# Performance work log

Hardware: AMD Instinct MI355X
Metric: run time of the kernel (lower is better)

Reference implementation:

```python
import jax, jax.numpy as jnp
import numpy as np
import math

# ---- config (YOLOv3 / 416, COCO) ----
ANCS_SCALE = np.array([[0.024,0.031],[0.038,0.072],[0.079,0.055],
                       [0.072,0.147],[0.149,0.108],[0.142,0.286],
                       [0.279,0.216],[0.375,0.476],[0.897,0.784]], dtype=np.float32)
NUMS_CENG = [2704, 676, 169]          # 52^2, 26^2, 13^2
NUMS_ANC = [3, 3, 3]
NUM_CLASSES = 80
LOSS_WEIGHT = [1.0, 1.0, 1.0]
B, NGT = 32, 20
HWA = sum(NUMS_CENG) * 3              # 10647
GDIM = 1 + NUM_CLASSES + 4 + 1 + 4    # conf + cls + txywh + weight + ltrb
FP16_EPS = 0.0009765625               # torch.finfo(float16).eps
BCE_EPS = 1e-6
GRIDS = [int(math.sqrt(n)) for n in NUMS_CENG]          # [52, 26, 13]
OFFS = [int(x) for x in np.cumsum([0] + NUMS_CENG)[:3]]  # layer offsets in cells


def ltrb2xywh(b):
    return jnp.concatenate([(b[..., :2] + b[..., 2:]) * 0.5, b[..., 2:] - b[..., :2]], axis=-1)


def x_bce(p, g):
    p = jnp.clip(p, BCE_EPS, 1.0 - BCE_EPS)
    return -(g * jnp.log(p) + (1.0 - g) * jnp.log(1.0 - p))


def fmatch4yolov3(gb_ltrb, glabels):
    """gb_ltrb [NGT,4] float, glabels [NGT] int -> g_yolo_one [HWA,GDIM].
    Faithful to the torch code, including the (buggy) inner loop over ALL
    GTs' best-anchor ids for each GT i, and the write order (-1 ignore first,
    positive row overwrite after), replicated via a sequential lax.scan."""
    ancs = jnp.asarray(ANCS_SCALE)
    gxywh = ltrb2xywh(gb_ltrb)
    wh = gxywh[:, 2:]                                     # [NGT,2]
    # wh-only IoU (boxes concentric at origin)
    inter = jnp.minimum(wh[:, None, 0], ancs[None, :, 0]) * jnp.minimum(wh[:, None, 1], ancs[None, :, 1])
    union = wh.prod(-1)[:, None] + ancs.prod(-1)[None, :] - inter
    ids_p_anc = jnp.argmax(inter / union, axis=-1).astype(jnp.int32)  # [NGT]
    weights = 2.0 - wh.prod(-1)
    onehot = jax.nn.one_hot(glabels - 1, NUM_CLASSES, dtype=gb_ltrb.dtype)
    g0 = jnp.zeros((HWA, GDIM), dtype=gb_ltrb.dtype)
    neg = jnp.full((3, 1), -1.0, dtype=gb_ltrb.dtype)

    def step(g, p):
        i = p // NGT            # GT whose cxy / wh / label are used
        k = p % NGT             # GT whose best anchor id is used
        cxy = gxywh[i, :2]
        a = ids_p_anc[k]
        ceng = a // NUMS_ANC[0]
        for j in range(3):      # static loop over the 3 layers
            grid, off = GRIDS[j], OFFS[j]
            colrow = (cxy * grid).astype(jnp.int32)       # [col,row]
            idx = (off + colrow[1] * grid + colrow[0]) * 3
            # ignore: conf=-1 for all 3 anchors of this cell
            g = jax.lax.dynamic_update_slice(g, neg, (idx, 0))
            # candidate positive row for this layer
            txy = (cxy - colrow.astype(cxy.dtype) / grid) * grid
            twh = jnp.log(wh[i] / ancs[a])
            t = jnp.concatenate([jnp.ones((1,), cxy.dtype), onehot[i], txy, twh,
                                 weights[i][None], gb_ltrb[i]])     # [GDIM]
            pidx = idx + (a % NUMS_ANC[j])
            cur = jax.lax.dynamic_slice(g, (pidx, 0), (1, GDIM))
            g = jax.lax.dynamic_update_slice(g, jnp.where(ceng == j, t[None, :], cur), (pidx, 0))
        return g, None

    g, _ = jax.lax.scan(step, g0, jnp.arange(NGT * NGT, dtype=jnp.int32))
    return g


def _forward(pconf, pcls, ptxywh, gboxes_ltrb, glabels):
    gyolos = jax.lax.stop_gradient(jax.vmap(fmatch4yolov3)(gboxes_ltrb, glabels))  # [B,HWA,GDIM]
    s_ = 1 + NUM_CLASSES
    gconf = gyolos[:, :, 0]
    mask_pos = (gconf > 0).astype(pconf.dtype)
    mask_neg = (gconf == 0).astype(pconf.dtype)
    nums_pos = jnp.clip(mask_pos.sum(-1), FP16_EPS, None)
    # cls loss (BCE on sigmoid, pos cells only)
    lv = x_bce(jax.nn.sigmoid(pcls), gyolos[:, :, 1:s_])
    l_cls = ((lv.sum(-1) * mask_pos).sum(-1) / nums_pos).mean() * LOSS_WEIGHT[2]
    # conf loss (MSE on sigmoid, masked means)
    pconf_sig = jax.nn.sigmoid(pconf).reshape(pconf.shape[0], -1)
    lv = (pconf_sig - gconf) ** 2
    l_conf_pos = (lv * mask_pos).sum() / mask_pos.sum() * LOSS_WEIGHT[0] * 30
    l_conf_neg = (lv * mask_neg).sum() / mask_neg.sum() * LOSS_WEIGHT[1] * 30
    # box loss: xy BCE, wh MSE, weighted by (2 - w*h)
    weight = gyolos[:, :, s_ + 4]
    lv = x_bce(jax.nn.sigmoid(ptxywh[:, :, :2]), gyolos[:, :, s_:s_ + 2])
    l_txty = ((lv.sum(-1) * mask_pos * weight).sum(-1) / nums_pos).mean()
    lv = (ptxywh[:, :, 2:4] - gyolos[:, :, s_ + 2:s_ + 4]) ** 2
    l_twth = ((lv.sum(-1) * mask_pos * weight).sum(-1) / nums_pos).mean()
    return l_conf_pos + l_conf_neg + l_cls + l_txty + l_twth


def setup_inputs() -> dict:
    key = jax.random.key(0)
    k1, k2, k3, k4, k5, k6 = jax.random.split(key, 6)
    pconf = jax.random.normal(k1, (B, HWA, 1), dtype=jnp.float32)
    pcls = jax.random.normal(k2, (B, HWA, NUM_CLASSES), dtype=jnp.float32)
    ptxywh = jax.random.normal(k3, (B, HWA, 4), dtype=jnp.float32)
    cxy = jax.random.uniform(k4, (B, NGT, 2), minval=0.2, maxval=0.8)
    wh = jax.random.uniform(k5, (B, NGT, 2), minval=0.05, maxval=0.3)
    gboxes_ltrb = jnp.concatenate([cxy - wh * 0.5, cxy + wh * 0.5], axis=-1)
    glabels = jax.random.randint(k6, (B, NGT), 1, NUM_CLASSES + 1, dtype=jnp.int32)
    return {"pconf": pconf, "pcls": pcls, "ptxywh": ptxywh,
            "gboxes_ltrb": gboxes_ltrb, "glabels": glabels}


def reference(pconf, pcls, ptxywh, gboxes_ltrb, glabels):
    return _forward(pconf, pcls, ptxywh, gboxes_ltrb, glabels)
```

## Files before the change

### kernel.cpp

```cpp
#include <hip/hip_runtime.h>
#include <math.h>

#define BATCH 32
#define NSLICE 16
#define SLICE_LEN 666
#define NGT 20
#define HWA 10647
#define NCLS 80
#define FP16_EPS 0.0009765625f
#define BCE_EPS 1e-6f

__device__ __constant__ float ANCS[9][2] = {
    {0.024f, 0.031f}, {0.038f, 0.072f}, {0.079f, 0.055f},
    {0.072f, 0.147f}, {0.149f, 0.108f}, {0.142f, 0.286f},
    {0.279f, 0.216f}, {0.375f, 0.476f}, {0.897f, 0.784f}};

__device__ __forceinline__ float flog(float x) { return __logf(x); }
__device__ __forceinline__ float fsig(float x) {
  return __builtin_amdgcn_rcpf(1.0f + __expf(-x));
}


__global__ __launch_bounds__(256) void yolo_main(
    const float* __restrict__ pconf,
    const float* __restrict__ pcls,
    const float* __restrict__ ptxywh,
    const float* __restrict__ gbox,
    const int* __restrict__ glab,
    float* __restrict__ part)
{
  const int b = blockIdx.x;
  const int sl = blockIdx.y;
  const int tid = threadIdx.x;
  const int r0 = sl * SLICE_LEN;
  const int r1 = min(r0 + SLICE_LEN, HWA);

  __shared__ int cell[SLICE_LEN];
  __shared__ int pos_list[256];
  __shared__ float s_cx[NGT], s_cy[NGT], s_w[NGT], s_h[NGT], s_wt[NGT];
  __shared__ int s_a[NGT], s_lab[NGT], s_idx[NGT][3];
  __shared__ int s_np;
  __shared__ float red[4][8];

  for (int r = tid; r < SLICE_LEN; r += 256) cell[r] = 0;
  if (tid == 0) s_np = 0;
  if (tid < NGT) {
    const float* gb = gbox + (b * NGT + tid) * 4;
    float l = gb[0], t = gb[1], r = gb[2], bo = gb[3];
    float cx = (l + r) * 0.5f, cy = (t + bo) * 0.5f;
    float w = r - l, h = bo - t;
    s_cx[tid] = cx; s_cy[tid] = cy; s_w[tid] = w; s_h[tid] = h;
    s_wt[tid] = 2.0f - w * h;
    s_lab[tid] = glab[b * NGT + tid];
    float best = -1e30f; int bi = 0;
    for (int a = 0; a < 9; ++a) {
      float inter = fminf(w, ANCS[a][0]) * fminf(h, ANCS[a][1]);
      float uni = w * h + ANCS[a][0] * ANCS[a][1] - inter;
      float ratio = inter / uni;
      if (ratio > best) { best = ratio; bi = a; }
    }
    s_a[tid] = bi;
    const int GR[3] = {52, 26, 13};
    const int OF[3] = {0, 2704, 3380};
    for (int j = 0; j < 3; ++j) {
      int col = (int)(cx * (float)GR[j]);
      int row = (int)(cy * (float)GR[j]);
      s_idx[tid][j] = (OF[j] + row * GR[j] + col) * 3;
    }
  }
  __syncthreads();

  for (int p = tid; p < NGT * NGT; p += 256) {
    int i = p / NGT, k = p - i * NGT;
    int a = s_a[k];
    int ceng = a / 3;
    int pn = (2 * p + 1) << 16;
    int pp = ((2 * p + 2) << 16) | (1 << 15) | (i * 9 + a);
    for (int j = 0; j < 3; ++j) {
      int idx = s_idx[i][j];
      if (idx + 2 >= r0 && idx < r1) {
#pragma unroll
        for (int d = 0; d < 3; ++d) {
          int t = idx + d;
          if (t >= r0 && t < r1) atomicMax(&cell[t - r0], pn);
        }
      }
      if (ceng == j) {
        int t = idx + (a - ceng * 3);
        if (t >= r0 && t < r1) atomicMax(&cell[t - r0], pp);
      }
    }
  }
  __syncthreads();

  float sum_pos = 0.f, sum_neg = 0.f;
  int cnt_pos = 0, cnt_neg = 0;
  for (int r = r0 + tid; r < r1; r += 256) {
    int c = cell[r - r0];
    float x = pconf[(size_t)b * HWA + r];
    float s = fsig(x);
    if (c == 0) {
      sum_neg += s * s; cnt_neg++;
    } else if (c & (1 << 15)) {
      float d = s - 1.0f; sum_pos += d * d; cnt_pos++;
      int slot = atomicAdd(&s_np, 1);
      if (slot < 256) pos_list[slot] = ((c & 0xFF) << 16) | r;
    }
  }
  __syncthreads();
  int P = s_np;

  float cls_sum = 0.f;
  for (int idx = tid; idx < P * NCLS; idx += 256) {
    int pr = idx / NCLS, c = idx - pr * NCLS;
    int pk = pos_list[pr];
    int r = pk & 0xFFFF, rec = pk >> 16;
    int i = rec / 9;
    int lab = s_lab[i] - 1;
    float x = pcls[((size_t)b * HWA + r) * NCLS + c];
    float s = fsig(x);
    s = fminf(fmaxf(s, BCE_EPS), 1.0f - BCE_EPS);
    float g = (c == lab) ? 1.0f : 0.0f;
    cls_sum += -(g * flog(s) + (1.0f - g) * flog(1.0f - s));
  }

  float txty_sum = 0.f, twth_sum = 0.f;
  for (int q = tid; q < P; q += 256) {
    int pk = pos_list[q];
    int r = pk & 0xFFFF, rec = pk >> 16;
    int i = rec / 9, a = rec - i * 9;
    int ceng = a / 3;
    const int GR[3] = {52, 26, 13};
    float grid = (float)GR[ceng];
    float cx = s_cx[i], cy = s_cy[i];
    int col = (int)(cx * grid), row = (int)(cy * grid);
    float tx = (cx - (float)col / grid) * grid;
    float ty = (cy - (float)row / grid) * grid;
    float twx = flog(s_w[i] / ANCS[a][0]);
    float twy = flog(s_h[i] / ANCS[a][1]);
    float wgt = s_wt[i];
    const float* pt = ptxywh + ((size_t)b * HWA + r) * 4;
    float s0 = fsig(pt[0]);
    float s1 = fsig(pt[1]);
    s0 = fminf(fmaxf(s0, BCE_EPS), 1.0f - BCE_EPS);
    s1 = fminf(fmaxf(s1, BCE_EPS), 1.0f - BCE_EPS);
    float b0 = -(tx * flog(s0) + (1.0f - tx) * flog(1.0f - s0));
    float b1 = -(ty * flog(s1) + (1.0f - ty) * flog(1.0f - s1));
    txty_sum += (b0 + b1) * wgt;
    float d2 = pt[2] - twx, d3 = pt[3] - twy;
    twth_sum += (d2 * d2 + d3 * d3) * wgt;
  }

  float v[7] = {sum_pos, sum_neg, cls_sum, txty_sum, twth_sum,
                (float)cnt_pos, (float)cnt_neg};
  int lane = tid & 63, wv = tid >> 6;
  for (int m = 0; m < 7; ++m) {
    float x = v[m];
    for (int o = 32; o > 0; o >>= 1) x += __shfl_down(x, o, 64);
    if (lane == 0) red[wv][m] = x;
  }
  __syncthreads();
  if (tid == 0) {
    float* w = part + (b * NSLICE + sl) * 8;
    for (int m = 0; m < 7; ++m)
      w[m] = red[0][m] + red[1][m] + red[2][m] + red[3][m];
  }
}

__global__ __launch_bounds__(512) void yolo_final(
    const float* __restrict__ part, float* __restrict__ out) {
  const int t = threadIdx.x;
  __shared__ float sb[BATCH][8];
  float v[7];
  const float* w = part + t * 8;
#pragma unroll
  for (int m = 0; m < 7; ++m) v[m] = w[m];
#pragma unroll
  for (int o = 8; o > 0; o >>= 1)
#pragma unroll
    for (int m = 0; m < 7; ++m) v[m] += __shfl_down(v[m], o, 16);
  if ((t & 15) == 0) {
    int b = t >> 4;
    float np = fmaxf(v[5], FP16_EPS);
    float rnp = 1.0f / np;
    sb[b][0] = v[0];
    sb[b][1] = v[1];
    sb[b][2] = v[5];
    sb[b][3] = v[6];
    sb[b][4] = v[2] * rnp;
    sb[b][5] = v[3] * rnp;
    sb[b][6] = v[4] * rnp;
  }
  __syncthreads();
  if (t < 32) {
    float u[7];
#pragma unroll
    for (int m = 0; m < 7; ++m) u[m] = sb[t][m];
#pragma unroll
    for (int o = 16; o > 0; o >>= 1)
#pragma unroll
      for (int m = 0; m < 7; ++m) u[m] += __shfl_down(u[m], o, 32);
    if (t == 0) {
      out[0] = u[0] / u[2] * 30.0f + u[1] / u[3] * 30.0f +
               (u[4] + u[5] + u[6]) * (1.0f / (float)BATCH);
    }
  }
}

extern "C" void kernel_launch(void* const* d_in, const int* in_sizes, int n_in,
                              void* d_out, int out_size, void* d_ws,
                              size_t ws_size, hipStream_t stream) {
  const float* pconf  = (const float*)d_in[0];
  const float* pcls   = (const float*)d_in[1];
  const float* ptxywh = (const float*)d_in[2];
  const float* gbox   = (const float*)d_in[3];
  const int*   glab   = (const int*)d_in[4];
  float* part = (float*)d_ws;

  dim3 grid(BATCH, NSLICE);
  yolo_main<<<grid, 256, 0, stream>>>(pconf, pcls, ptxywh, gbox, glab, part);
  yolo_final<<<1, 512, 0, stream>>>(part, (float*)d_out);
}
```

Measured before the change: 153.3 us.

## Split dense negative-conf sum into separate blocks and match once per batch

Computes the negative-confidence term as a dense vectorized sum of squared sigmoids over all pconf, minus a correction over matched cells. Anchor matching is done once per batch item in a single block holding the full cell map in shared memory, instead of being repeated per slice. This is meant to remove redundant matching work and make the pconf pass bandwidth-friendly. The cost is large shared-memory use and long serial per-batch blocks. The final kernel is reworked to combine the dense partials with the per-batch results.

```diff
diff --git a/kernel.cpp b/kernel.cpp
--- a/kernel.cpp
+++ b/kernel.cpp
@@ -2,11 +2,12 @@
 #include <math.h>
 
 #define BATCH 32
-#define NSLICE 16
-#define SLICE_LEN 666
 #define NGT 20
 #define HWA 10647
 #define NCLS 80
+#define NMATCH 32
+#define NDENSE 333
+#define TOT_F4 ((BATCH * HWA) / 4)
 #define FP16_EPS 0.0009765625f
 #define BCE_EPS 1e-6f
 
@@ -29,21 +30,39 @@
     const int* __restrict__ glab,
     float* __restrict__ part)
 {
-  const int b = blockIdx.x;
-  const int sl = blockIdx.y;
   const int tid = threadIdx.x;
-  const int r0 = sl * SLICE_LEN;
-  const int r1 = min(r0 + SLICE_LEN, HWA);
-
-  __shared__ int cell[SLICE_LEN];
+  const int blk = blockIdx.x;
+
+  __shared__ int cell[HWA];
   __shared__ int pos_list[256];
+  __shared__ int special[256];
   __shared__ float s_cx[NGT], s_cy[NGT], s_w[NGT], s_h[NGT], s_wt[NGT];
   __shared__ int s_a[NGT], s_lab[NGT], s_idx[NGT][3];
-  __shared__ int s_np;
+  __shared__ int s_np, s_nsp;
   __shared__ float red[4][8];
 
-  for (int r = tid; r < SLICE_LEN; r += 256) cell[r] = 0;
-  if (tid == 0) s_np = 0;
+  if (blk >= NMATCH) {
+    int f = (blk - NMATCH) * 256 + tid;
+    float sum = 0.f;
+    if (f < TOT_F4) {
+      float4 v = ((const float4*)pconf)[f];
+      float s0 = fsig(v.x), s1 = fsig(v.y), s2 = fsig(v.z), s3 = fsig(v.w);
+      sum = s0 * s0 + s1 * s1 + s2 * s2 + s3 * s3;
+    }
+    int lane = tid & 63, wv = tid >> 6;
+    for (int o = 32; o > 0; o >>= 1) sum += __shfl_down(sum, o, 64);
+    if (lane == 0) red[wv][0] = sum;
+    __syncthreads();
+    if (tid == 0)
+      part[8 * NMATCH + (blk - NMATCH)] =
+          red[0][0] + red[1][0] + red[2][0] + red[3][0];
+    return;
+  }
+
+  const int b = blk;
+
+  for (int r = tid; r < HWA; r += 256) cell[r] = 0;
+  if (tid == 0) { s_np = 0; s_nsp = 0; }
   if (tid < NGT) {
     const float* gb = gbox + (b * NGT + tid) * 4;
     float l = gb[0], t = gb[1], r = gb[2], bo = gb[3];
@@ -78,37 +97,40 @@
     int pp = ((2 * p + 2) << 16) | (1 << 15) | (i * 9 + a);
     for (int j = 0; j < 3; ++j) {
       int idx = s_idx[i][j];
-      if (idx + 2 >= r0 && idx < r1) {
-#pragma unroll
-        for (int d = 0; d < 3; ++d) {
-          int t = idx + d;
-          if (t >= r0 && t < r1) atomicMax(&cell[t - r0], pn);
-        }
+      atomicMax(&cell[idx], pn);
+      atomicMax(&cell[idx + 1], pn);
+      atomicMax(&cell[idx + 2], pn);
+      if (ceng == j) atomicMax(&cell[idx + (a - ceng * 3)], pp);
+    }
+  }
+  __syncthreads();
+
+  for (int r = tid; r < HWA; r += 256) {
+    int c = cell[r];
+    if (c != 0) {
+      int slot = atomicAdd(&s_nsp, 1);
+      int pk = ((c & 0xFF) << 16) | r;
+      if (c & (1 << 15)) {
+        pk |= (int)0x80000000;
+        int ps = atomicAdd(&s_np, 1);
+        pos_list[ps] = ((c & 0xFF) << 16) | r;
       }
-      if (ceng == j) {
-        int t = idx + (a - ceng * 3);
-        if (t >= r0 && t < r1) atomicMax(&cell[t - r0], pp);
-      }
-    }
-  }
-  __syncthreads();
-
-  float sum_pos = 0.f, sum_neg = 0.f;
-  int cnt_pos = 0, cnt_neg = 0;
-  for (int r = r0 + tid; r < r1; r += 256) {
-    int c = cell[r - r0];
-    float x = pconf[(size_t)b * HWA + r];
-    float s = fsig(x);
-    if (c == 0) {
-      sum_neg += s * s; cnt_neg++;
-    } else if (c & (1 << 15)) {
-      float d = s - 1.0f; sum_pos += d * d; cnt_pos++;
-      int slot = atomicAdd(&s_np, 1);
-      if (slot < 256) pos_list[slot] = ((c & 0xFF) << 16) | r;
-    }
-  }
-  __syncthreads();
-  int P = s_np;
+      special[slot] = pk;
+    }
+  }
+  __syncthreads();
+  const int NSP = s_nsp, P = s_np;
+
+  float possum = 0.f, negcorr = 0.f; int cnt_pos = 0;
+  for (int q = tid; q < NSP; q += 256) {
+    int pk = special[q];
+    int r = pk & 0xFFFF;
+    float s = fsig(pconf[(size_t)b * HWA + r]);
+    negcorr += s * s;
+    if (pk < 0) {
+      float d = s - 1.0f; possum += d * d; cnt_pos++;
+    }
+  }
 
   float cls_sum = 0.f;
   for (int idx = tid; idx < P * NCLS; idx += 256) {
@@ -151,59 +173,66 @@
     twth_sum += (d2 * d2 + d3 * d3) * wgt;
   }
 
-  float v[7] = {sum_pos, sum_neg, cls_sum, txty_sum, twth_sum,
-                (float)cnt_pos, (float)cnt_neg};
+  float v[6] = {possum, negcorr, (float)cnt_pos, cls_sum, txty_sum, twth_sum};
   int lane = tid & 63, wv = tid >> 6;
-  for (int m = 0; m < 7; ++m) {
+  for (int m = 0; m < 6; ++m) {
     float x = v[m];
     for (int o = 32; o > 0; o >>= 1) x += __shfl_down(x, o, 64);
     if (lane == 0) red[wv][m] = x;
   }
   __syncthreads();
   if (tid == 0) {
-    float* w = part + (b * NSLICE + sl) * 8;
-    for (int m = 0; m < 7; ++m)
-      w[m] = red[0][m] + red[1][m] + red[2][m] + red[3][m];
+    float t[6];
+    for (int m = 0; m < 6; ++m)
+      t[m] = red[0][m] + red[1][m] + red[2][m] + red[3][m];
+    float np = fmaxf(t[2], FP16_EPS);
+    float rnp = 1.0f / np;
+    float* w = part + b * 8;
+    w[0] = t[0];
+    w[1] = t[1];
+    w[2] = t[2];
+    w[3] = (float)NSP;
+    w[4] = t[3] * rnp;
+    w[5] = t[4] * rnp;
+    w[6] = t[5] * rnp;
   }
 }
 
 __global__ __launch_bounds__(512) void yolo_final(
     const float* __restrict__ part, float* __restrict__ out) {
   const int t = threadIdx.x;
-  __shared__ float sb[BATCH][8];
-  float v[7];
-  const float* w = part + t * 8;
-#pragma unroll
-  for (int m = 0; m < 7; ++m) v[m] = w[m];
-#pragma unroll
-  for (int o = 8; o > 0; o >>= 1)
-#pragma unroll
-    for (int m = 0; m < 7; ++m) v[m] += __shfl_down(v[m], o, 16);
-  if ((t & 15) == 0) {
-    int b = t >> 4;
-    float np = fmaxf(v[5], FP16_EPS);
-    float rnp = 1.0f / np;
-    sb[b][0] = v[0];
-    sb[b][1] = v[1];
-    sb[b][2] = v[5];
-    sb[b][3] = v[6];
-    sb[b][4] = v[2] * rnp;
-    sb[b][5] = v[3] * rnp;
-    sb[b][6] = v[4] * rnp;
-  }
-  __syncthreads();
-  if (t < 32) {
-    float u[7];
-#pragma unroll
-    for (int m = 0; m < 7; ++m) u[m] = sb[t][m];
-#pragma unroll
-    for (int o = 16; o > 0; o >>= 1)
-#pragma unroll
-      for (int m = 0; m < 7; ++m) u[m] += __shfl_down(u[m], o, 32);
-    if (t == 0) {
-      out[0] = u[0] / u[2] * 30.0f + u[1] / u[3] * 30.0f +
-               (u[4] + u[5] + u[6]) * (1.0f / (float)BATCH);
-    }
+  float acc[8];
+#pragma unroll
+  for (int m = 0; m < 8; ++m) acc[m] = 0.f;
+  if (t < NDENSE) acc[0] = part[8 * NMATCH + t];
+  if (t < NMATCH) {
+    const float* w = part + t * 8;
+#pragma unroll
+    for (int m = 0; m < 7; ++m) acc[m + 1] = w[m];
+  }
+  __shared__ float red[8][8];
+  int lane = t & 63, wv = t >> 6;
+#pragma unroll
+  for (int m = 0; m < 8; ++m) {
+    float x = acc[m];
+    for (int o = 32; o > 0; o >>= 1) x += __shfl_down(x, o, 64);
+    if (lane == 0) red[wv][m] = x;
+  }
+  __syncthreads();
+  if (t == 0) {
+    float s[8];
+#pragma unroll
+    for (int m = 0; m < 8; ++m) {
+      float x = 0.f;
+      for (int w2 = 0; w2 < 8; ++w2) x += red[w2][m];
+      s[m] = x;
+    }
+    float dense = s[0], possum = s[1], negcorr = s[2];
+    float cntpos = s[3], nsp = s[4];
+    float sum_neg = dense - negcorr;
+    float cnt_neg = (float)(BATCH * HWA) - nsp;
+    out[0] = possum / cntpos * 30.0f + sum_neg / cnt_neg * 30.0f +
+             (s[5] + s[6] + s[7]) * (1.0f / (float)BATCH);
   }
 }
 
@@ -217,7 +246,7 @@
   const int*   glab   = (const int*)d_in[4];
   float* part = (float*)d_ws;
 
-  dim3 grid(BATCH, NSLICE);
-  yolo_main<<<grid, 256, 0, stream>>>(pconf, pcls, ptxywh, gbox, glab, part);
+  yolo_main<<<dim3(NMATCH + NDENSE), 256, 0, stream>>>(
+      pconf, pcls, ptxywh, gbox, glab, part);
   yolo_final<<<1, 512, 0, stream>>>(part, (float*)d_out);
 }
```

Result: slower. 158.4 us (+3.3%).
